# Kernel optimization log

Measured on AMD Instinct MI355X. Metric: run time of the kernel, lower is better.

Reference implementation:

```python
import math
import jax, jax.numpy as jnp
import numpy as np

BATCH, SEQ, DIM, VOCAB = 8, 8192, 512, 44


def _positional_encoding(max_len, d):
    # sinusoidal PE identical to the torch module
    pos = jnp.arange(max_len, dtype=jnp.float32)[:, None]            # [L,1]
    div = jnp.exp(jnp.arange(0, d, 2, dtype=jnp.float32) * (-math.log(10000.0) / d))
    pe = jnp.zeros((max_len, d), dtype=jnp.float32)
    pe = pe.at[:, 0::2].set(jnp.sin(pos * div))
    pe = pe.at[:, 1::2].set(jnp.cos(pos * div))
    return pe


def _segment_ids(tokens):
    # tokens: [L] int. Reproduces _detect_event_changes with a lax.scan
    # carrying note_counter; segment id = cumulative count of change points.
    cur, prev = tokens[1:], tokens[:-1]

    def step(nc, cp):
        c, p = cp
        nc = jnp.where((c >= 36) & (c <= 41), jnp.int32(2), nc)
        is_note = c < 12
        change = jnp.where(is_note, (p >= 12) | (nc > 0), p < 12)
        nc = jnp.where(is_note, nc - 1, nc)
        return nc, change

    _, changes = jax.lax.scan(step, jnp.int32(0), (cur, prev))
    flags = jnp.concatenate([jnp.zeros((1,), jnp.int32), changes.astype(jnp.int32)])
    return jnp.cumsum(flags)  # [L]


def setup_inputs() -> dict:
    key = jax.random.key(0)
    k1, k2 = jax.random.split(key)
    input_tokens = jax.random.randint(k1, (BATCH, SEQ), 0, VOCAB, dtype=jnp.int64)
    emb_table = jax.random.normal(k2, (VOCAB, DIM), dtype=jnp.float32)  # nn.init.normal_
    return {"input_tokens": input_tokens, "emb_table": emb_table}


def reference(input_tokens, emb_table):
    d = emb_table.shape[1]
    seg = jax.vmap(_segment_ids)(input_tokens)          # [B,L] event index per token
    pe = _positional_encoding(input_tokens.shape[1], d) # enough rows: changes+1 <= L
    out = emb_table[input_tokens] * jnp.sqrt(jnp.float32(d)) + pe[seg]
    return out  # dropout p=0.0 (eval) -> identity
```

## Files before the change

### kernel.cpp

```cpp
#include <hip/hip_runtime.h>
#include <hip/hip_bf16.h>

#define BATCH 8
#define SEQ   8192
#define DIM   512

typedef float f32x4 __attribute__((ext_vector_type(4)));

#define INV2PI   0.15915494309189535f
#define SQRT_DIM 22.62741699796952f
#define C2 (-0.05190512648261504f)

#define SEG_BYTES ((size_t)BATCH * SEQ * 4)

#define TPB_PREP  1024
#define SEG_CHUNK (SEQ / TPB_PREP)
#define NWAVE     (TPB_PREP / 64)

#define TIX(k) ((k) + ((k) >> 3))

__global__ __launch_bounds__(TPB_PREP)
void seg_kernel(const int* __restrict__ tok, int* __restrict__ seg) {
    __shared__ int s_tok[SEQ + SEQ / 8];
    __shared__ int s_seg[SEQ + SEQ / 8];
    __shared__ int s_pr[NWAVE], s_pv[NWAVE], s_cnt[NWAVE];

    const int tid  = threadIdx.x;
    const int lane = tid & 63;
    const int wv   = tid >> 6;

    const int b  = blockIdx.x;
    const int* t = tok + (size_t)b * SEQ;
    int*      sg = seg + (size_t)b * SEQ;

    #pragma unroll
    for (int m = 0; m < SEG_CHUNK; ++m) {
        const int k = m * TPB_PREP + tid;
        s_tok[TIX(k)] = t[k];
    }
    __syncthreads();

    const int start = tid * SEG_CHUNK;
    const int end   = start + SEG_CHUNK;
    const int lo    = (start < 1) ? 1 : start;

    int reset = 0, val = 0;
    #pragma unroll
    for (int i = lo; i < end; ++i) {
        const int c = s_tok[TIX(i)];
        if (c >= 36 && c <= 41) { reset = 1; val = 2; }
        if (c < 12) val -= 1;
    }

    int ir = reset, iv = val;
    #pragma unroll
    for (int off = 1; off < 64; off <<= 1) {
        const int pv = __shfl_up(iv, off);
        const int pr = __shfl_up(ir, off);
        if (lane >= off && !ir) { iv += pv; ir = pr; }
    }
    int er = __shfl_up(ir, 1), ev = __shfl_up(iv, 1);
    if (lane == 0) { er = 0; ev = 0; }
    if (lane == 63) { s_pr[wv] = ir; s_pv[wv] = iv; }
    __syncthreads();
    int bv = 0;
    for (int w = 0; w < wv; ++w) {
        if (s_pr[w]) bv = s_pv[w]; else bv += s_pv[w];
    }
    const int nc_entry = er ? ev : (bv + ev);

    int nc = nc_entry, total = 0;
    #pragma unroll
    for (int i = lo; i < end; ++i) {
        const int c = s_tok[TIX(i)];
        const int p = s_tok[TIX(i - 1)];
        if (c >= 36 && c <= 41) nc = 2;
        const bool is_note = (c < 12);
        const int f = is_note ? (int)((p >= 12) || (nc > 0)) : (int)(p < 12);
        if (is_note) nc -= 1;
        total += f;
    }

    int it = total;
    #pragma unroll
    for (int off = 1; off < 64; off <<= 1) {
        const int pv = __shfl_up(it, off);
        if (lane >= off) it += pv;
    }
    int et = __shfl_up(it, 1);
    if (lane == 0) et = 0;
    if (lane == 63) s_cnt[wv] = it;
    __syncthreads();
    int boff = 0;
    for (int w = 0; w < wv; ++w) boff += s_cnt[w];
    int run = boff + et;

    nc = nc_entry;
    if (start == 0) s_seg[TIX(0)] = 0;
    #pragma unroll
    for (int i = lo; i < end; ++i) {
        const int c = s_tok[TIX(i)];
        const int p = s_tok[TIX(i - 1)];
        if (c >= 36 && c <= 41) nc = 2;
        const bool is_note = (c < 12);
        const int f = is_note ? (int)((p >= 12) || (nc > 0)) : (int)(p < 12);
        if (is_note) nc -= 1;
        run += f;
        s_seg[TIX(i)] = run;
    }
    __syncthreads();
    #pragma unroll
    for (int m = 0; m < SEG_CHUNK; ++m) {
        const int k = m * TPB_PREP + tid;
        sg[k] = s_seg[TIX(k)];
    }
}

#define OUT_BLOCKS ((BATCH * SEQ) / 4)

__global__ __launch_bounds__(256)
void out_kernel(const int*   __restrict__ tok,
                const int*   __restrict__ seg,
                const float* __restrict__ emb,
                float*       __restrict__ out) {
    const int bid = (int)blockIdx.x;
    const int vb  = ((bid & 7) << 11) | (bid >> 3);

    const int lane = (int)threadIdx.x & 63;
    const int row  = __builtin_amdgcn_readfirstlane(
                        vb * 4 + ((int)threadIdx.x >> 6));

    const int   token = tok[row];
    const float segf  = (float)seg[row];

    const int dA = lane << 2;
    const int dB = dA + 256;

    const float* erow = emb + (size_t)token * DIM;
    const f32x4 eA = *reinterpret_cast<const f32x4*>(erow + dA);
    const f32x4 eB = *reinterpret_cast<const f32x4*>(erow + dB);

    float vA[4], vB[4];
    #pragma unroll
    for (int j = 0; j < 2; ++j) {
        const float kA = (float)((dA >> 1) + j);
        float rA = segf * __builtin_amdgcn_exp2f(C2 * kA) * INV2PI;
        rA -= floorf(rA);
        vA[2 * j]     = __builtin_amdgcn_sinf(rA);
        vA[2 * j + 1] = __builtin_amdgcn_cosf(rA);

        const float kB = (float)((dB >> 1) + j);
        float rB = segf * __builtin_amdgcn_exp2f(C2 * kB) * INV2PI;
        rB -= floorf(rB);
        vB[2 * j]     = __builtin_amdgcn_sinf(rB);
        vB[2 * j + 1] = __builtin_amdgcn_cosf(rB);
    }

    f32x4 oA, oB;
    oA.x = eA.x * SQRT_DIM + vA[0];  oA.y = eA.y * SQRT_DIM + vA[1];
    oA.z = eA.z * SQRT_DIM + vA[2];  oA.w = eA.w * SQRT_DIM + vA[3];
    oB.x = eB.x * SQRT_DIM + vB[0];  oB.y = eB.y * SQRT_DIM + vB[1];
    oB.z = eB.z * SQRT_DIM + vB[2];  oB.w = eB.w * SQRT_DIM + vB[3];

    float* orow = out + (size_t)row * DIM;
    __builtin_nontemporal_store(oA, reinterpret_cast<f32x4*>(orow + dA));
    __builtin_nontemporal_store(oB, reinterpret_cast<f32x4*>(orow + dB));
}

extern "C" void kernel_launch(void* const* d_in, const int* in_sizes, int n_in,
                              void* d_out, int out_size, void* d_ws, size_t ws_size,
                              hipStream_t stream) {
    const int*   tok = (const int*)d_in[0];
    const float* emb = (const float*)d_in[1];
    float*       out = (float*)d_out;
    int*         seg = (int*)d_ws;

    seg_kernel<<<BATCH, TPB_PREP, 0, stream>>>(tok, seg);
    out_kernel<<<OUT_BLOCKS, 256, 0, stream>>>(tok, seg, emb, out);
}
```

Measured before the change: 35.96 us.

## Keep segment-scan tokens in registers with 256-thread blocks and vector loads

The segment-id kernel drops its shared-memory staging of tokens and segment ids. Each of 256 threads now loads its 32-token chunk straight into registers with int4 loads and keeps per-element prefix counts in registers. It then writes the results with int4 stores, using a two-pass scan over the chunk instead of three. This removes LDS traffic and a barrier, but uses fewer threads per batch row and more registers per thread, so the serial per-thread chain is four times longer.

Result: faster. 34.28 us (-4.7%).

```diff
diff --git a/kernel.cpp b/kernel.cpp
--- a/kernel.cpp
+++ b/kernel.cpp
@@ -13,43 +13,43 @@
 
 #define SEG_BYTES ((size_t)BATCH * SEQ * 4)
 
-#define TPB_PREP  1024
-#define SEG_CHUNK (SEQ / TPB_PREP)
-#define NWAVE     (TPB_PREP / 64)
+#define SEG_TPB 256
+#define SCHUNK  (SEQ / SEG_TPB)
 
-#define TIX(k) ((k) + ((k) >> 3))
+__global__ __launch_bounds__(SEG_TPB)
+void seg_kernel(const int* __restrict__ tok, int* __restrict__ seg) {
+    __shared__ int s_r[4], s_v[4], s_c[4];
 
-__global__ __launch_bounds__(TPB_PREP)
-void seg_kernel(const int* __restrict__ tok, int* __restrict__ seg) {
-    __shared__ int s_tok[SEQ + SEQ / 8];
-    __shared__ int s_seg[SEQ + SEQ / 8];
-    __shared__ int s_pr[NWAVE], s_pv[NWAVE], s_cnt[NWAVE];
-
-    const int tid  = threadIdx.x;
+    const int tid  = (int)threadIdx.x;
     const int lane = tid & 63;
     const int wv   = tid >> 6;
+    const int b    = (int)blockIdx.x;
+    const int* t   = tok + (size_t)b * SEQ;
+    int*      sg   = seg + (size_t)b * SEQ;
 
-    const int b  = blockIdx.x;
-    const int* t = tok + (size_t)b * SEQ;
-    int*      sg = seg + (size_t)b * SEQ;
+    const int start = tid * SCHUNK;
 
+    int4 tt[8];
     #pragma unroll
-    for (int m = 0; m < SEG_CHUNK; ++m) {
-        const int k = m * TPB_PREP + tid;
-        s_tok[TIX(k)] = t[k];
+    for (int m = 0; m < 8; ++m)
+        tt[m] = *reinterpret_cast<const int4*>(t + start + m * 4);
+
+    const int pentry = (start > 0) ? t[start - 1] : 0;
+
+    int c[SCHUNK];
+    #pragma unroll
+    for (int m = 0; m < 8; ++m) {
+        c[4 * m + 0] = tt[m].x;  c[4 * m + 1] = tt[m].y;
+        c[4 * m + 2] = tt[m].z;  c[4 * m + 3] = tt[m].w;
     }
-    __syncthreads();
-
-    const int start = tid * SEG_CHUNK;
-    const int end   = start + SEG_CHUNK;
-    const int lo    = (start < 1) ? 1 : start;
 
     int reset = 0, val = 0;
     #pragma unroll
-    for (int i = lo; i < end; ++i) {
-        const int c = s_tok[TIX(i)];
-        if (c >= 36 && c <= 41) { reset = 1; val = 2; }
-        if (c < 12) val -= 1;
+    for (int i = 0; i < SCHUNK; ++i) {
+        if (i == 0 && start == 0) continue;
+        const int cc = c[i];
+        if (cc >= 36 && cc <= 41) { reset = 1; val = 2; }
+        if (cc < 12) val -= 1;
     }
 
     int ir = reset, iv = val;
@@ -61,27 +61,34 @@
     }
     int er = __shfl_up(ir, 1), ev = __shfl_up(iv, 1);
     if (lane == 0) { er = 0; ev = 0; }
-    if (lane == 63) { s_pr[wv] = ir; s_pv[wv] = iv; }
+    if (lane == 63) { s_r[wv] = ir; s_v[wv] = iv; }
     __syncthreads();
     int bv = 0;
-    for (int w = 0; w < wv; ++w) {
-        if (s_pr[w]) bv = s_pv[w]; else bv += s_pv[w];
+    #pragma unroll
+    for (int w = 0; w < 4; ++w) {
+        if (w < wv) { if (s_r[w]) bv = s_v[w]; else bv += s_v[w]; }
     }
     const int nc_entry = er ? ev : (bv + ev);
 
-    int nc = nc_entry, total = 0;
+    int nc = nc_entry, cum = 0;
+    int pref[SCHUNK];
+    int p = pentry;
     #pragma unroll
-    for (int i = lo; i < end; ++i) {
-        const int c = s_tok[TIX(i)];
-        const int p = s_tok[TIX(i - 1)];
-        if (c >= 36 && c <= 41) nc = 2;
-        const bool is_note = (c < 12);
-        const int f = is_note ? (int)((p >= 12) || (nc > 0)) : (int)(p < 12);
-        if (is_note) nc -= 1;
-        total += f;
+    for (int i = 0; i < SCHUNK; ++i) {
+        const int cc = c[i];
+        int f = 0;
+        if (!(i == 0 && start == 0)) {
+            if (cc >= 36 && cc <= 41) nc = 2;
+            const bool is_note = (cc < 12);
+            f = is_note ? (int)((p >= 12) || (nc > 0)) : (int)(p < 12);
+            if (is_note) nc -= 1;
+        }
+        cum += f;
+        pref[i] = cum;
+        p = cc;
     }
 
-    int it = total;
+    int it = cum;
     #pragma unroll
     for (int off = 1; off < 64; off <<= 1) {
         const int pv = __shfl_up(it, off);
@@ -89,30 +96,23 @@
     }
     int et = __shfl_up(it, 1);
     if (lane == 0) et = 0;
-    if (lane == 63) s_cnt[wv] = it;
+    if (lane == 63) s_c[wv] = it;
     __syncthreads();
     int boff = 0;
-    for (int w = 0; w < wv; ++w) boff += s_cnt[w];
-    int run = boff + et;
+    #pragma unroll
+    for (int w = 0; w < 4; ++w) {
+        if (w < wv) boff += s_c[w];
+    }
+    const int run = boff + et;
 
-    nc = nc_entry;
-    if (start == 0) s_seg[TIX(0)] = 0;
     #pragma unroll
-    for (int i = lo; i < end; ++i) {
-        const int c = s_tok[TIX(i)];
-        const int p = s_tok[TIX(i - 1)];
-        if (c >= 36 && c <= 41) nc = 2;
-        const bool is_note = (c < 12);
-        const int f = is_note ? (int)((p >= 12) || (nc > 0)) : (int)(p < 12);
-        if (is_note) nc -= 1;
-        run += f;
-        s_seg[TIX(i)] = run;
-    }
-    __syncthreads();
-    #pragma unroll
-    for (int m = 0; m < SEG_CHUNK; ++m) {
-        const int k = m * TPB_PREP + tid;
-        sg[k] = s_seg[TIX(k)];
+    for (int m = 0; m < 8; ++m) {
+        int4 o;
+        o.x = run + pref[4 * m + 0];
+        o.y = run + pref[4 * m + 1];
+        o.z = run + pref[4 * m + 2];
+        o.w = run + pref[4 * m + 3];
+        *reinterpret_cast<int4*>(sg + start + m * 4) = o;
     }
 }
 
@@ -175,6 +175,6 @@
     float*       out = (float*)d_out;
     int*         seg = (int*)d_ws;
 
-    seg_kernel<<<BATCH, TPB_PREP, 0, stream>>>(tok, seg);
+    seg_kernel<<<BATCH, SEG_TPB, 0, stream>>>(tok, seg);
     out_kernel<<<OUT_BLOCKS, 256, 0, stream>>>(tok, seg, emb, out);
 }
```
